# Optimization experiments

Measured on AMD Instinct MI355X. Metric: run time of the kernel, lower is better.

The kernel has to match this reference:

```python
import jax, jax.numpy as jnp
import numpy as np
import math

B, S, H, NH, HD, RD, INNER, MAXPOS, EPS = 2, 2048, 4096, 16, 256, 64, 16384, 2048, 1e-5


def setup_inputs() -> dict:
    key = jax.random.key(0)
    ks = jax.random.split(key, 8)
    sd = 0.02
    return {
        "hidden_states": jax.random.normal(ks[0], (B, S, H), jnp.float32),
        "attention_mask": jnp.ones((B, S), jnp.int32),
        "position_ids": jnp.broadcast_to(jnp.arange(S, dtype=jnp.int32), (B, S)),
        "ln_scale": jnp.ones((H,), jnp.float32),
        "ln_bias": jnp.zeros((H,), jnp.float32),
        "wq": jax.random.normal(ks[1], (H, H), jnp.float32) * sd,
        "wk": jax.random.normal(ks[2], (H, H), jnp.float32) * sd,
        "wv": jax.random.normal(ks[3], (H, H), jnp.float32) * sd,
        "wo": jax.random.normal(ks[4], (H, H), jnp.float32) * sd,
        "w_in": jax.random.normal(ks[5], (H, INNER), jnp.float32) * sd,
        "b_in": jnp.zeros((INNER,), jnp.float32),
        "w_out": jax.random.normal(ks[6], (INNER, H), jnp.float32) * sd,
        "b_out": jnp.zeros((H,), jnp.float32),
    }


def _rotate_every_two(t):
    # interleave (-odd, even) pairs along last dim
    r = jnp.stack((-t[..., 1::2], t[..., ::2]), axis=-1)
    return r.reshape(t.shape)


def reference(hidden_states, attention_mask, position_ids, ln_scale, ln_bias,
              wq, wk, wv, wo, w_in, b_in, w_out, b_out):
    x = hidden_states
    # LayerNorm (single ln feeds both attn and mlp in GPT-J parallel block)
    mu = jnp.mean(x, axis=-1, keepdims=True)
    var = jnp.mean(jnp.square(x - mu), axis=-1, keepdims=True)
    h = (x - mu) * jax.lax.rsqrt(var + EPS) * ln_scale + ln_bias

    # QKV projections (no bias), split heads: [B,S,NH,HD]
    q = (h @ wq).reshape(B, S, NH, HD)
    k = (h @ wk).reshape(B, S, NH, HD)
    v = (h @ wv).reshape(B, S, NH, HD)

    # sinusoidal table over rotary_dim, gathered by position_ids
    pos = jnp.arange(MAXPOS, dtype=jnp.float32)
    inv_freq = 1.0 / (10000.0 ** (jnp.arange(0, RD, 2, dtype=jnp.float32) / RD))
    freqs = pos[:, None] * inv_freq[None, :]          # [MAXPOS, RD//2]
    table = jnp.concatenate([jnp.sin(freqs), jnp.cos(freqs)], axis=-1)  # [MAXPOS, RD]
    sincos = table[position_ids]                      # [B,S,RD]
    sin, cos = jnp.split(sincos, 2, axis=-1)          # each [B,S,RD//2]
    sinr = jnp.repeat(sin[:, :, None, :], 2, axis=3)  # [B,S,1,RD]
    cosr = jnp.repeat(cos[:, :, None, :], 2, axis=3)

    def rope(t):
        return t * cosr + _rotate_every_two(t) * sinr

    q = jnp.concatenate([rope(q[..., :RD]), q[..., RD:]], axis=-1)
    k = jnp.concatenate([rope(k[..., :RD]), k[..., RD:]], axis=-1)

    # combined causal + padding mask -> additive bias
    causal = jnp.tril(jnp.ones((S, S), dtype=bool))
    mask = (attention_mask[:, None, None, :] > 0) & causal[None, None, :, :]
    bias = jnp.where(mask, 0.0, jnp.finfo(jnp.float32).min)  # [B,1,S,S]

    scale = 1.0 / math.sqrt(HD)
    scores = jnp.einsum('bqhd,bkhd->bhqk', q, k) * scale + bias
    attn = jax.nn.softmax(scores, axis=-1)
    ctx = jnp.einsum('bhqk,bkhd->bqhd', attn, v).reshape(B, S, H)
    attn_out = ctx @ wo

    # MLP on the same LN output (parallel residual), gelu_new ~ tanh gelu
    mlp = jax.nn.gelu(h @ w_in + b_in, approximate=True) @ w_out + b_out

    return x + attn_out + mlp
```

## Files before the change

### kernel.cpp

```cpp
#include <hip/hip_runtime.h>
#include <hip/hip_bf16.h>
#include <math.h>

namespace {

constexpr int kB = 2;
constexpr int kS = 2048;
constexpr int kH = 4096;
constexpr int kNH = 16;
constexpr int kHD = 256;

typedef __attribute__((ext_vector_type(4))) float f32x4;
typedef __attribute__((ext_vector_type(8))) short bf16x8;

__device__ __forceinline__ unsigned short f2bf(float f) {
  unsigned int u = __float_as_uint(f);
  u += 0x7FFFu + ((u >> 16) & 1u);
  return (unsigned short)(u >> 16);
}
__device__ __forceinline__ float bf2f(unsigned short h) {
  return __uint_as_float(((unsigned int)h) << 16);
}
__device__ __forceinline__ void gl2lds16(const void* g, void* l) {
  __builtin_amdgcn_global_load_lds(
      (const __attribute__((address_space(1))) unsigned int*)g,
      (__attribute__((address_space(3))) unsigned int*)l, 16, 0, 0);
}

__global__ __launch_bounds__(256) void ln_fwd(
    const float* __restrict__ x, const float* __restrict__ gam,
    const float* __restrict__ bet, unsigned short* __restrict__ hout,
    float* __restrict__ outp) {
  int row = blockIdx.x;
  int t = threadIdx.x;
  const float4* xr = (const float4*)(x + (size_t)row * kH);
  float4 v[4];
  float sum = 0.f, sq = 0.f;
#pragma unroll
  for (int i = 0; i < 4; i++) {
    v[i] = xr[t + i * 256];
    sum += v[i].x + v[i].y + v[i].z + v[i].w;
    sq += v[i].x * v[i].x + v[i].y * v[i].y + v[i].z * v[i].z + v[i].w * v[i].w;
  }
#pragma unroll
  for (int o = 32; o > 0; o >>= 1) {
    sum += __shfl_xor(sum, o);
    sq += __shfl_xor(sq, o);
  }
  __shared__ float red[8];
  if ((t & 63) == 0) { red[t >> 6] = sum; red[4 + (t >> 6)] = sq; }
  __syncthreads();
  sum = red[0] + red[1] + red[2] + red[3];
  sq = red[4] + red[5] + red[6] + red[7];
  float mu = sum * (1.f / kH);
  float rstd = rsqrtf(sq * (1.f / kH) - mu * mu + 1e-5f);
  const float4* gp = (const float4*)gam;
  const float4* bp = (const float4*)bet;
  ushort4* hr = (ushort4*)(hout + (size_t)row * kH);
  float4* orow = (float4*)(outp + (size_t)row * kH);
#pragma unroll
  for (int i = 0; i < 4; i++) {
    float4 g = gp[t + i * 256];
    float4 bb = bp[t + i * 256];
    ushort4 hv;
    hv.x = f2bf((v[i].x - mu) * rstd * g.x + bb.x);
    hv.y = f2bf((v[i].y - mu) * rstd * g.y + bb.y);
    hv.z = f2bf((v[i].z - mu) * rstd * g.z + bb.z);
    hv.w = f2bf((v[i].w - mu) * rstd * g.w + bb.w);
    hr[t + i * 256] = hv;
    orow[t + i * 256] = v[i];
  }
}

__global__ __launch_bounds__(256) void cvt_t(
    const float* __restrict__ in, int ldin, unsigned short* __restrict__ outp,
    int ldout) {
  __shared__ float tile[32][33];
  int n0 = blockIdx.x * 32, k0 = blockIdx.y * 32;
  int tx = threadIdx.x, ty = threadIdx.y;
#pragma unroll
  for (int i = 0; i < 4; i++)
    tile[ty + i * 8][tx] = in[(size_t)(k0 + ty + i * 8) * ldin + n0 + tx];
  __syncthreads();
#pragma unroll
  for (int i = 0; i < 4; i++)
    outp[(size_t)(n0 + ty + i * 8) * ldout + k0 + tx] =
        f2bf(tile[tx][ty + i * 8]);
}

__global__ __launch_bounds__(256) void vtrans(
    const unsigned short* __restrict__ v, unsigned short* __restrict__ vt) {
  __shared__ unsigned short tile[32][33];
  int bh = blockIdx.z;
  int s0 = blockIdx.x * 32, d0 = blockIdx.y * 32;
  int tx = threadIdx.x, ty = threadIdx.y;
  int b = bh >> 4, h = bh & 15;
  const unsigned short* src = v + (size_t)(b * kS) * kH + h * kHD;
#pragma unroll
  for (int i = 0; i < 4; i++)
    tile[ty + i * 8][tx] = src[(size_t)(s0 + ty + i * 8) * kH + d0 + tx];
  __syncthreads();
  unsigned short* dst = vt + (size_t)bh * kHD * kS;
#pragma unroll
  for (int i = 0; i < 4; i++)
    dst[(size_t)(d0 + ty + i * 8) * kS + s0 + tx] = tile[tx][ty + i * 8];
}

__global__ __launch_bounds__(256) void rope_scale(
    unsigned short* __restrict__ q, unsigned short* __restrict__ k,
    const int* __restrict__ pos) {
  int idx = blockIdx.x * 256 + threadIdx.x;
  int j = idx & 127;
  int rowh = idx >> 7;
  int h = rowh & 15;
  int s = (rowh >> 4) & 2047;
  int b = rowh >> 15;
  size_t off = ((size_t)(b * kS + s)) * kH + h * kHD + 2 * j;
  const float SCALE = 0.0625f;
  if (j < 32) {
    int p = pos[b * kS + s];
    float inv = exp2f(-(float)j * (13.287712379549449f / 32.f));
    float fr = (float)p * inv;
    float sn, cs;
    sincosf(fr, &sn, &cs);
    float e = bf2f(q[off]), o = bf2f(q[off + 1]);
    q[off] = f2bf((e * cs - o * sn) * SCALE);
    q[off + 1] = f2bf((o * cs + e * sn) * SCALE);
    e = bf2f(k[off]); o = bf2f(k[off + 1]);
    k[off] = f2bf(e * cs - o * sn);
    k[off + 1] = f2bf(o * cs + e * sn);
  } else {
    q[off] = f2bf(bf2f(q[off]) * SCALE);
    q[off + 1] = f2bf(bf2f(q[off + 1]) * SCALE);
  }
}

#define AF_MMA(P)                                                           \
  {                                                                         \
    bf16x8 af_[2][2];                                                       \
    _Pragma("unroll") for (int fm = 0; fm < 2; fm++)                        \
        _Pragma("unroll") for (int kk = 0; kk < 2; kk++) {                  \
      int q_ = (2 * (P) + fm) * 16 + l15;                                   \
      af_[fm][kk] = *(const bf16x8*)(cur + ((q_ & 64) << 8) + wm * 8192 +   \
                                     ((q_ & 63) << 7) +                     \
                                     ((((kk << 2) | l4) ^ key) << 4));      \
    }                                                                       \
    __builtin_amdgcn_s_setprio(1);                                          \
    _Pragma("unroll") for (int fm = 0; fm < 2; fm++)                        \
        _Pragma("unroll") for (int fn = 0; fn < 4; fn++)                    \
            _Pragma("unroll") for (int kk = 0; kk < 2; kk++)                \
      acc[2 * (P) + fm][fn] = __builtin_amdgcn_mfma_f32_16x16x32_bf16(      \
          af_[fm][kk], bfr[fn][kk], acc[2 * (P) + fm][fn], 0, 0, 0);        \
    __builtin_amdgcn_s_setprio(0);                                          \
  }

template <int EPI>
__global__ __launch_bounds__(512, 2) void gemm256(
    const unsigned short* __restrict__ A, int lda,
    const unsigned short* __restrict__ Bt, int ldb, void* __restrict__ Cp,
    int ldc, const float* __restrict__ bias, int K, int gx) {
  __shared__ __align__(16) char lds[131072];
  const int t = threadIdx.x;
  const int lane = t & 63, w = t >> 6;
  const int wm = w >> 2, wn = w & 3;
  const int l15 = lane & 15, l4 = lane >> 4;
  const int key = l15 & 7;

  const int nwg = gridDim.x;
  const int orig = blockIdx.x;
  const int wg = (orig & 7) * (nwg >> 3) + (orig >> 3);
  const int bx = wg % gx, by = wg / gx;
  const int m0 = by * 256, n0 = bx * 256;

  const int lr = t >> 3, ch = t & 7;
  const int swk = (ch ^ (lr & 7)) * 8;
  const unsigned short* aE0 = A + (size_t)(m0 + lr) * lda + swk;
  const unsigned short* aE1 = A + (size_t)(m0 + 128 + lr) * lda + swk;
  const unsigned short* aL0 = A + (size_t)(m0 + 64 + lr) * lda + swk;
  const unsigned short* aL1 = A + (size_t)(m0 + 192 + lr) * lda + swk;
  const unsigned short* b00 = Bt + (size_t)(n0 + lr) * ldb + swk;
  const unsigned short* b01 = Bt + (size_t)(n0 + 64 + lr) * ldb + swk;
  const unsigned short* b10 = Bt + (size_t)(n0 + 128 + lr) * ldb + swk;
  const unsigned short* b11 = Bt + (size_t)(n0 + 192 + lr) * ldb + swk;
  const int t16 = t * 16;

  f32x4 acc[8][4];
#pragma unroll
  for (int m = 0; m < 8; m++)
#pragma unroll
    for (int n = 0; n < 4; n++) acc[m][n] = (f32x4)(0.f);

  {
    char* b = lds;
    gl2lds16(b00, b + 32768 + t16); b00 += 64;
    gl2lds16(b01, b + 40960 + t16); b01 += 64;
    gl2lds16(b10, b + 49152 + t16); b10 += 64;
    gl2lds16(b11, b + 57344 + t16); b11 += 64;
    gl2lds16(aE0, b + t16);         aE0 += 64;
    gl2lds16(aE1, b + 8192 + t16);  aE1 += 64;
    gl2lds16(aL0, b + 16384 + t16); aL0 += 64;
    gl2lds16(aL1, b + 24576 + t16); aL1 += 64;
  }
  asm volatile("s_waitcnt vmcnt(2)" ::: "memory");
  asm volatile("s_barrier" ::: "memory");

  const int nt = K >> 6;
  for (int kt = 0; kt < nt; ++kt) {
    const char* cur = lds + (kt & 1) * 65536;
    char* nxt = lds + (((kt & 1) ^ 1)) * 65536;
    const bool pre = (kt + 1 < nt);
    bf16x8 bfr[4][2];
    if (pre) {
      gl2lds16(b00, nxt + 32768 + t16); b00 += 64;
      gl2lds16(b01, nxt + 40960 + t16); b01 += 64;
      gl2lds16(b10, nxt + 49152 + t16); b10 += 64;
      gl2lds16(b11, nxt + 57344 + t16); b11 += 64;
    }
#pragma unroll
    for (int fn = 0; fn < 4; fn++)
#pragma unroll
      for (int kk = 0; kk < 2; kk++) {
        int n = wn * 64 + fn * 16 + l15;
        bfr[fn][kk] = *(const bf16x8*)(cur + 32768 + (n << 7) +
                                       ((((kk << 2) | l4) ^ key) << 4));
      }
    AF_MMA(0)
    if (pre) {
      gl2lds16(aE0, nxt + t16);         aE0 += 64;
      gl2lds16(aE1, nxt + 8192 + t16);  aE1 += 64;
      gl2lds16(aL0, nxt + 16384 + t16); aL0 += 64;
      gl2lds16(aL1, nxt + 24576 + t16); aL1 += 64;
    }
    AF_MMA(1)
    if (pre) asm volatile("s_waitcnt vmcnt(8)" ::: "memory");
    else     asm volatile("s_waitcnt vmcnt(0)" ::: "memory");
    asm volatile("s_barrier" ::: "memory");
    AF_MMA(2)
    AF_MMA(3)
    asm volatile("s_waitcnt lgkmcnt(0)" ::: "memory");
    if (pre) asm volatile("s_waitcnt vmcnt(2)" ::: "memory");
    asm volatile("s_barrier" ::: "memory");
  }

  const int crow = m0 + wm * 128 + l4 * 4;
  const int ccol = n0 + wn * 64 + l15;
#pragma unroll
  for (int m = 0; m < 8; m++) {
#pragma unroll
    for (int n = 0; n < 4; n++) {
      int col = ccol + n * 16;
#pragma unroll
      for (int r = 0; r < 4; r++) {
        int row = crow + m * 16 + r;
        float v = acc[m][n][r];
        size_t idx = (size_t)row * ldc + col;
        if constexpr (EPI == 0) {
          ((unsigned short*)Cp)[idx] = f2bf(v);
        } else if constexpr (EPI == 1) {
          float u = v + bias[col];
          float c = 0.7978845608028654f * (u + 0.044715f * u * u * u);
          float g = u / (1.0f + __expf(-2.0f * c));
          ((unsigned short*)Cp)[idx] = f2bf(g);
        } else if constexpr (EPI == 2) {
          ((float*)Cp)[idx] += v;
        } else {
          ((float*)Cp)[idx] += v + bias[col];
        }
      }
    }
  }
}

__global__ __launch_bounds__(512) void attn_fwd(
    const unsigned short* __restrict__ q, const unsigned short* __restrict__ k,
    const unsigned short* __restrict__ vt, const int* __restrict__ amask,
    unsigned short* __restrict__ ctx) {
  __shared__ __align__(16) char alds[147456];
  const int t = threadIdx.x, lane = t & 63, w = t >> 6;
  const int bid = blockIdx.x;
  const int qb = 15 - (bid >> 5);
  const int bh = bid & 31;
  const int b = bh >> 4, h = bh & 15;
  const int l15 = lane & 15, l4 = lane >> 4;
  const int qbase = qb * 128;

  bf16x8 qf[8];
  {
    int qrow = qbase + w * 16 + l15;
    const unsigned short* qp =
        q + (size_t)(b * kS + qrow) * kH + h * kHD + l4 * 8;
#pragma unroll
    for (int ks = 0; ks < 8; ks++) qf[ks] = *(const bf16x8*)(qp + ks * 32);
  }
  f32x4 o[16];
#pragma unroll
  for (int nf = 0; nf < 16; nf++) o[nf] = (f32x4)(0.f);
  float mr[4] = {-INFINITY, -INFINITY, -INFINITY, -INFINITY};
  float lr[4] = {0.f, 0.f, 0.f, 0.f};

  const unsigned short* kbase = k + (size_t)(b * kS) * kH + h * kHD;
  const unsigned short* vbase = vt + (size_t)bh * kHD * kS;
  unsigned short* sPw = (unsigned short*)(alds + 131072 + w * 2048);
  const int nt = 2 * qb + 2;

  const int krow = t >> 5, kch = t & 31;
  const int kcs = (kch ^ (krow & 7)) * 8;
  const int vrow = t >> 3, vch = t & 7;
  const int vcs = (vch ^ (vrow & 7)) * 8;
  const int t16b = t * 16;

#define ATTN_STAGE(KV0, BUF)                                                 \
  {                                                                          \
    char* kd = alds + (BUF) * 32768;                                         \
    char* vd = alds + 65536 + (BUF) * 32768;                                 \
    _Pragma("unroll") for (int i = 0; i < 4; i++) {                          \
      gl2lds16(kbase + (size_t)((KV0) + krow + i * 16) * kH + kcs,           \
               kd + i * 8192 + t16b);                                        \
      gl2lds16(vbase + (size_t)(vrow + i * 64) * kS + (KV0) + vcs,           \
               vd + i * 8192 + t16b);                                        \
    }                                                                        \
  }

  ATTN_STAGE(0, 0)

  for (int kvt = 0; kvt < nt; kvt++) {
    const int kv0 = kvt * 64;
    const int cb = kvt & 1;
    if (kvt + 1 < nt) {
      ATTN_STAGE(kv0 + 64, cb ^ 1)
      asm volatile("s_waitcnt vmcnt(8)" ::: "memory");
    } else {
      asm volatile("s_waitcnt vmcnt(0)" ::: "memory");
    }
    asm volatile("s_barrier" ::: "memory");

    const unsigned short* sK = (const unsigned short*)(alds + cb * 32768);
    const unsigned short* sV =
        (const unsigned short*)(alds + 65536 + cb * 32768);

    f32x4 sc[4];
#pragma unroll
    for (int g = 0; g < 4; g++) sc[g] = (f32x4)(0.f);
    __builtin_amdgcn_s_setprio(1);
#pragma unroll
    for (int g = 0; g < 4; g++) {
      int row = g * 16 + l15;
#pragma unroll
      for (int ks = 0; ks < 8; ks++) {
        bf16x8 kf =
            *(const bf16x8*)&sK[row * 256 + (((ks * 4 + l4) ^ (row & 7)) * 8)];
        sc[g] = __builtin_amdgcn_mfma_f32_16x16x32_bf16(qf[ks], kf, sc[g], 0, 0, 0);
      }
    }
    __builtin_amdgcn_s_setprio(0);

    int am[4];
#pragma unroll
    for (int g = 0; g < 4; g++) am[g] = amask[b * kS + kv0 + g * 16 + l15];
    float mx[4];
#pragma unroll
    for (int r = 0; r < 4; r++) {
      int qi = qbase + w * 16 + l4 * 4 + r;
      float a = -INFINITY;
#pragma unroll
      for (int g = 0; g < 4; g++) {
        bool ok = (kv0 + g * 16 + l15 <= qi) && (am[g] != 0);
        float s = ok ? sc[g][r] : -INFINITY;
        sc[g][r] = s;
        a = fmaxf(a, s);
      }
#pragma unroll
      for (int d = 1; d < 16; d <<= 1) a = fmaxf(a, __shfl_xor(a, d));
      mx[r] = a;
    }
    bool nd = false;
#pragma unroll
    for (int r = 0; r < 4; r++) nd |= (mx[r] > mr[r] + 8.f);
    if (__any(nd)) {
#pragma unroll
      for (int r = 0; r < 4; r++) {
        float nm = fmaxf(mr[r], mx[r]);
        float c = __expf(mr[r] - nm);
        lr[r] *= c;
        mr[r] = nm;
#pragma unroll
        for (int nf = 0; nf < 16; nf++) o[nf][r] *= c;
      }
    }
#pragma unroll
    for (int r = 0; r < 4; r++) {
      int prow = l4 * 4 + r;
      int pkey = (prow ^ (prow >> 2)) & 7;
      float rs = 0.f;
#pragma unroll
      for (int g = 0; g < 4; g++) {
        float p = __expf(sc[g][r] - mr[r]);
        rs += p;
        int kvl = g * 16 + l15;
        sPw[prow * 64 + (((kvl >> 3) ^ pkey) << 3) + (kvl & 7)] = f2bf(p);
      }
#pragma unroll
      for (int d = 1; d < 16; d <<= 1) rs += __shfl_xor(rs, d);
      lr[r] += rs;
    }
    asm volatile("s_waitcnt lgkmcnt(0)" ::: "memory");

    int rkey = (l15 ^ (l15 >> 2)) & 7;
    bf16x8 pa[2];
#pragma unroll
    for (int ks2 = 0; ks2 < 2; ks2++)
      pa[ks2] = *(const bf16x8*)&sPw[l15 * 64 + (((ks2 * 4 + l4) ^ rkey) << 3)];
    __builtin_amdgcn_s_setprio(1);
#pragma unroll
    for (int nf = 0; nf < 16; nf++) {
      int vr = nf * 16 + l15;
#pragma unroll
      for (int ks2 = 0; ks2 < 2; ks2++) {
        bf16x8 vf =
            *(const bf16x8*)&sV[vr * 64 + (((ks2 * 4 + l4) ^ (vr & 7)) * 8)];
        o[nf] = __builtin_amdgcn_mfma_f32_16x16x32_bf16(pa[ks2], vf, o[nf], 0, 0, 0);
      }
    }
    __builtin_amdgcn_s_setprio(0);
    asm volatile("s_barrier" ::: "memory");
  }

  float invl[4];
#pragma unroll
  for (int r = 0; r < 4; r++) invl[r] = 1.0f / lr[r];
#pragma unroll
  for (int nf = 0; nf < 16; nf++) {
    int d = nf * 16 + l15;
#pragma unroll
    for (int r = 0; r < 4; r++) {
      int qi = qbase + w * 16 + l4 * 4 + r;
      ctx[(size_t)(b * kS + qi) * kH + h * kHD + d] = f2bf(o[nf][r] * invl[r]);
    }
  }
#undef ATTN_STAGE
}

}

extern "C" void kernel_launch(void* const* d_in, const int* in_sizes, int n_in,
                              void* d_out, int out_size, void* d_ws,
                              size_t ws_size, hipStream_t stream) {
  const float* x = (const float*)d_in[0];
  const int* amask = (const int*)d_in[1];
  const int* pos = (const int*)d_in[2];
  const float* lns = (const float*)d_in[3];
  const float* lnb = (const float*)d_in[4];
  const float* wq = (const float*)d_in[5];
  const float* wk = (const float*)d_in[6];
  const float* wv = (const float*)d_in[7];
  const float* wo = (const float*)d_in[8];
  const float* w_in = (const float*)d_in[9];
  const float* b_in = (const float*)d_in[10];
  const float* w_out = (const float*)d_in[11];
  const float* b_out = (const float*)d_in[12];
  float* out = (float*)d_out;

  if (ws_size < 268435456ull) return;
  char* ws = (char*)d_ws;
  unsigned short* h_bf = (unsigned short*)ws;
  unsigned short* big = (unsigned short*)(ws + 33554432ull);
  unsigned short* vbuf = (unsigned short*)(ws + 167772160ull);
  unsigned short* wbuf = (unsigned short*)(ws + 201326592ull);
  unsigned short* mid = big;
  unsigned short* qbuf = big;
  unsigned short* kbuf = big + 16777216;
  unsigned short* vtb = big + 33554432;
  unsigned short* ctxb = vbuf;

  dim3 t256(256);
  dim3 t512(512);
  dim3 t32x8(32, 8);

  ln_fwd<<<kB * kS, t256, 0, stream>>>(x, lns, lnb, h_bf, out);

  for (int c = 0; c < 2; c++) {
    cvt_t<<<dim3(256, 128), t32x8, 0, stream>>>(w_in + c * 8192, 16384, wbuf, 4096);
    gemm256<1><<<dim3(512), t512, 0, stream>>>(
        h_bf, 4096, wbuf, 4096, mid + c * 8192, 16384, b_in + c * 8192, 4096, 32);
  }
  for (int c = 0; c < 2; c++) {
    cvt_t<<<dim3(128, 256), t32x8, 0, stream>>>(
        w_out + (size_t)c * 8192 * 4096, 4096, wbuf, 8192);
    if (c == 0)
      gemm256<3><<<dim3(256), t512, 0, stream>>>(mid + c * 8192, 16384, wbuf,
                                                 8192, out, 4096, b_out, 8192, 16);
    else
      gemm256<2><<<dim3(256), t512, 0, stream>>>(
          mid + c * 8192, 16384, wbuf, 8192, out, 4096, nullptr, 8192, 16);
  }

  const float* wqkv[3] = {wq, wk, wv};
  unsigned short* qkvp[3] = {qbuf, kbuf, vbuf};
  for (int i = 0; i < 3; i++) {
    cvt_t<<<dim3(128, 128), t32x8, 0, stream>>>(wqkv[i], 4096, wbuf, 4096);
    gemm256<0><<<dim3(256), t512, 0, stream>>>(h_bf, 4096, wbuf, 4096,
                                               qkvp[i], 4096, nullptr, 4096, 16);
  }
  rope_scale<<<32768, t256, 0, stream>>>(qbuf, kbuf, pos);
  vtrans<<<dim3(64, 8, 32), t32x8, 0, stream>>>(vbuf, vtb);
  attn_fwd<<<dim3(512), t512, 0, stream>>>(qbuf, kbuf, vtb, amask, ctxb);
  cvt_t<<<dim3(128, 128), t32x8, 0, stream>>>(wo, 4096, wbuf, 4096);
  gemm256<2><<<dim3(256), t512, 0, stream>>>(ctxb, 4096, wbuf, 4096, out,
                                             4096, nullptr, 4096, 16);
}
```

Before: 2.005 ms.

## Replace 256x256 GEMM with 256x128 tile, K=32 triple-buffered pipeline

Rewrites the bf16 MFMA GEMM to use 256x128 output tiles with a 32-wide K step and a three-stage LDS ring buffer loaded via global_load_lds. The wave layout becomes 4x2, each wave holding a 4x4 accumulator grid, and LDS drops to about 72KB so four blocks can target each CU. All GEMM launches double their grid counts to match. The aim is more occupancy, more blocks per GEMM and deeper prefetch; in exchange, operand reuse per tile is lower and there is a barrier every 32-wide K step.

```diff
diff --git a/kernel.cpp b/kernel.cpp
--- a/kernel.cpp
+++ b/kernel.cpp
@@ -26,6 +26,9 @@
       (const __attribute__((address_space(1))) unsigned int*)g,
       (__attribute__((address_space(3))) unsigned int*)l, 16, 0, 0);
 }
+
+#define SBAR asm volatile("s_barrier" ::: "memory")
+#define LGKM0 asm volatile("s_waitcnt lgkmcnt(0)" ::: "memory")
 
 __global__ __launch_bounds__(256) void ln_fwd(
     const float* __restrict__ x, const float* __restrict__ gam,
@@ -135,117 +138,88 @@
   }
 }
 
-#define AF_MMA(P)                                                           \
-  {                                                                         \
-    bf16x8 af_[2][2];                                                       \
-    _Pragma("unroll") for (int fm = 0; fm < 2; fm++)                        \
-        _Pragma("unroll") for (int kk = 0; kk < 2; kk++) {                  \
-      int q_ = (2 * (P) + fm) * 16 + l15;                                   \
-      af_[fm][kk] = *(const bf16x8*)(cur + ((q_ & 64) << 8) + wm * 8192 +   \
-                                     ((q_ & 63) << 7) +                     \
-                                     ((((kk << 2) | l4) ^ key) << 4));      \
-    }                                                                       \
-    __builtin_amdgcn_s_setprio(1);                                          \
-    _Pragma("unroll") for (int fm = 0; fm < 2; fm++)                        \
-        _Pragma("unroll") for (int fn = 0; fn < 4; fn++)                    \
-            _Pragma("unroll") for (int kk = 0; kk < 2; kk++)                \
-      acc[2 * (P) + fm][fn] = __builtin_amdgcn_mfma_f32_16x16x32_bf16(      \
-          af_[fm][kk], bfr[fn][kk], acc[2 * (P) + fm][fn], 0, 0, 0);        \
-    __builtin_amdgcn_s_setprio(0);                                          \
-  }
-
 template <int EPI>
-__global__ __launch_bounds__(512, 2) void gemm256(
+__global__ __launch_bounds__(512, 4) void gemmk(
     const unsigned short* __restrict__ A, int lda,
     const unsigned short* __restrict__ Bt, int ldb, void* __restrict__ Cp,
     int ldc, const float* __restrict__ bias, int K, int gx) {
-  __shared__ __align__(16) char lds[131072];
+  __shared__ __align__(16) char lds[73728];
   const int t = threadIdx.x;
   const int lane = t & 63, w = t >> 6;
-  const int wm = w >> 2, wn = w & 3;
+  const int wm = w >> 1, wn = w & 1;
   const int l15 = lane & 15, l4 = lane >> 4;
-  const int key = l15 & 7;
 
   const int nwg = gridDim.x;
   const int orig = blockIdx.x;
   const int wg = (orig & 7) * (nwg >> 3) + (orig >> 3);
   const int bx = wg % gx, by = wg / gx;
-  const int m0 = by * 256, n0 = bx * 256;
-
-  const int lr = t >> 3, ch = t & 7;
-  const int swk = (ch ^ (lr & 7)) * 8;
-  const unsigned short* aE0 = A + (size_t)(m0 + lr) * lda + swk;
-  const unsigned short* aE1 = A + (size_t)(m0 + 128 + lr) * lda + swk;
-  const unsigned short* aL0 = A + (size_t)(m0 + 64 + lr) * lda + swk;
-  const unsigned short* aL1 = A + (size_t)(m0 + 192 + lr) * lda + swk;
-  const unsigned short* b00 = Bt + (size_t)(n0 + lr) * ldb + swk;
-  const unsigned short* b01 = Bt + (size_t)(n0 + 64 + lr) * ldb + swk;
-  const unsigned short* b10 = Bt + (size_t)(n0 + 128 + lr) * ldb + swk;
-  const unsigned short* b11 = Bt + (size_t)(n0 + 192 + lr) * ldb + swk;
+  const int m0 = by * 256, n0 = bx * 128;
+
+  const int lr = t >> 2, ch = t & 3;
+  const int swo = ((ch ^ ((lr & 3) ^ ((lr >> 2) & 3))) << 3);
+  const unsigned short* aS0 = A + (size_t)(m0 + lr) * lda + swo;
+  const unsigned short* aS1 = A + (size_t)(m0 + 128 + lr) * lda + swo;
+  const unsigned short* bS = Bt + (size_t)(n0 + lr) * ldb + swo;
   const int t16 = t * 16;
 
-  f32x4 acc[8][4];
-#pragma unroll
-  for (int m = 0; m < 8; m++)
+  const int keyR = (l15 & 3) ^ ((l15 >> 2) & 3);
+  const int rch = ((l4 ^ keyR) << 4);
+  const int abase = wm * 4096 + l15 * 64 + rch;
+  const int bbase = 16384 + wn * 4096 + l15 * 64 + rch;
+
+  f32x4 acc[4][4];
+#pragma unroll
+  for (int m = 0; m < 4; m++)
 #pragma unroll
     for (int n = 0; n < 4; n++) acc[m][n] = (f32x4)(0.f);
 
-  {
-    char* b = lds;
-    gl2lds16(b00, b + 32768 + t16); b00 += 64;
-    gl2lds16(b01, b + 40960 + t16); b01 += 64;
-    gl2lds16(b10, b + 49152 + t16); b10 += 64;
-    gl2lds16(b11, b + 57344 + t16); b11 += 64;
-    gl2lds16(aE0, b + t16);         aE0 += 64;
-    gl2lds16(aE1, b + 8192 + t16);  aE1 += 64;
-    gl2lds16(aL0, b + 16384 + t16); aL0 += 64;
-    gl2lds16(aL1, b + 24576 + t16); aL1 += 64;
-  }
-  asm volatile("s_waitcnt vmcnt(2)" ::: "memory");
-  asm volatile("s_barrier" ::: "memory");
-
-  const int nt = K >> 6;
+  gl2lds16(aS0, lds + t16);
+  gl2lds16(aS1, lds + 8192 + t16);
+  gl2lds16(bS, lds + 16384 + t16);
+  aS0 += 32; aS1 += 32; bS += 32;
+  gl2lds16(aS0, lds + 24576 + t16);
+  gl2lds16(aS1, lds + 24576 + 8192 + t16);
+  gl2lds16(bS, lds + 24576 + 16384 + t16);
+  aS0 += 32; aS1 += 32; bS += 32;
+  asm volatile("s_waitcnt vmcnt(3)" ::: "memory");
+  SBAR;
+
+  int offR = 0, off1 = 24576, offW = 49152;
+  const int nt = K >> 5;
   for (int kt = 0; kt < nt; ++kt) {
-    const char* cur = lds + (kt & 1) * 65536;
-    char* nxt = lds + (((kt & 1) ^ 1)) * 65536;
-    const bool pre = (kt + 1 < nt);
-    bf16x8 bfr[4][2];
-    if (pre) {
-      gl2lds16(b00, nxt + 32768 + t16); b00 += 64;
-      gl2lds16(b01, nxt + 40960 + t16); b01 += 64;
-      gl2lds16(b10, nxt + 49152 + t16); b10 += 64;
-      gl2lds16(b11, nxt + 57344 + t16); b11 += 64;
-    }
-#pragma unroll
-    for (int fn = 0; fn < 4; fn++)
-#pragma unroll
-      for (int kk = 0; kk < 2; kk++) {
-        int n = wn * 64 + fn * 16 + l15;
-        bfr[fn][kk] = *(const bf16x8*)(cur + 32768 + (n << 7) +
-                                       ((((kk << 2) | l4) ^ key) << 4));
-      }
-    AF_MMA(0)
-    if (pre) {
-      gl2lds16(aE0, nxt + t16);         aE0 += 64;
-      gl2lds16(aE1, nxt + 8192 + t16);  aE1 += 64;
-      gl2lds16(aL0, nxt + 16384 + t16); aL0 += 64;
-      gl2lds16(aL1, nxt + 24576 + t16); aL1 += 64;
-    }
-    AF_MMA(1)
-    if (pre) asm volatile("s_waitcnt vmcnt(8)" ::: "memory");
-    else     asm volatile("s_waitcnt vmcnt(0)" ::: "memory");
-    asm volatile("s_barrier" ::: "memory");
-    AF_MMA(2)
-    AF_MMA(3)
-    asm volatile("s_waitcnt lgkmcnt(0)" ::: "memory");
-    if (pre) asm volatile("s_waitcnt vmcnt(2)" ::: "memory");
-    asm volatile("s_barrier" ::: "memory");
-  }
-
-  const int crow = m0 + wm * 128 + l4 * 4;
+    if (kt + 2 < nt) {
+      gl2lds16(aS0, lds + offW + t16);
+      gl2lds16(aS1, lds + offW + 8192 + t16);
+      gl2lds16(bS, lds + offW + 16384 + t16);
+      aS0 += 32; aS1 += 32; bS += 32;
+    }
+    const char* cur = lds + offR;
+    bf16x8 af[4], bv[4];
+#pragma unroll
+    for (int m = 0; m < 4; m++)
+      af[m] = *(const bf16x8*)(cur + abase + m * 1024);
+#pragma unroll
+    for (int n = 0; n < 4; n++)
+      bv[n] = *(const bf16x8*)(cur + bbase + n * 1024);
+    __builtin_amdgcn_s_setprio(1);
+#pragma unroll
+    for (int m = 0; m < 4; m++)
+#pragma unroll
+      for (int n = 0; n < 4; n++)
+        acc[m][n] = __builtin_amdgcn_mfma_f32_16x16x32_bf16(af[m], bv[n],
+                                                            acc[m][n], 0, 0, 0);
+    __builtin_amdgcn_s_setprio(0);
+    LGKM0;
+    if (kt + 2 < nt) asm volatile("s_waitcnt vmcnt(3)" ::: "memory");
+    else             asm volatile("s_waitcnt vmcnt(0)" ::: "memory");
+    SBAR;
+    int tmp = offR; offR = off1; off1 = offW; offW = tmp;
+  }
+
+  const int crow = m0 + wm * 64 + l4 * 4;
   const int ccol = n0 + wn * 64 + l15;
 #pragma unroll
-  for (int m = 0; m < 8; m++) {
+  for (int m = 0; m < 4; m++) {
 #pragma unroll
     for (int n = 0; n < 4; n++) {
       int col = ccol + n * 16;
@@ -480,31 +454,31 @@
 
   for (int c = 0; c < 2; c++) {
     cvt_t<<<dim3(256, 128), t32x8, 0, stream>>>(w_in + c * 8192, 16384, wbuf, 4096);
-    gemm256<1><<<dim3(512), t512, 0, stream>>>(
-        h_bf, 4096, wbuf, 4096, mid + c * 8192, 16384, b_in + c * 8192, 4096, 32);
+    gemmk<1><<<dim3(1024), t512, 0, stream>>>(
+        h_bf, 4096, wbuf, 4096, mid + c * 8192, 16384, b_in + c * 8192, 4096, 64);
   }
   for (int c = 0; c < 2; c++) {
     cvt_t<<<dim3(128, 256), t32x8, 0, stream>>>(
         w_out + (size_t)c * 8192 * 4096, 4096, wbuf, 8192);
     if (c == 0)
-      gemm256<3><<<dim3(256), t512, 0, stream>>>(mid + c * 8192, 16384, wbuf,
-                                                 8192, out, 4096, b_out, 8192, 16);
+      gemmk<3><<<dim3(512), t512, 0, stream>>>(mid + c * 8192, 16384, wbuf,
+                                               8192, out, 4096, b_out, 8192, 32);
     else
-      gemm256<2><<<dim3(256), t512, 0, stream>>>(
-          mid + c * 8192, 16384, wbuf, 8192, out, 4096, nullptr, 8192, 16);
+      gemmk<2><<<dim3(512), t512, 0, stream>>>(
+          mid + c * 8192, 16384, wbuf, 8192, out, 4096, nullptr, 8192, 32);
   }
 
   const float* wqkv[3] = {wq, wk, wv};
   unsigned short* qkvp[3] = {qbuf, kbuf, vbuf};
   for (int i = 0; i < 3; i++) {
     cvt_t<<<dim3(128, 128), t32x8, 0, stream>>>(wqkv[i], 4096, wbuf, 4096);
-    gemm256<0><<<dim3(256), t512, 0, stream>>>(h_bf, 4096, wbuf, 4096,
-                                               qkvp[i], 4096, nullptr, 4096, 16);
+    gemmk<0><<<dim3(512), t512, 0, stream>>>(h_bf, 4096, wbuf, 4096,
+                                             qkvp[i], 4096, nullptr, 4096, 32);
   }
   rope_scale<<<32768, t256, 0, stream>>>(qbuf, kbuf, pos);
   vtrans<<<dim3(64, 8, 32), t32x8, 0, stream>>>(vbuf, vtb);
   attn_fwd<<<dim3(512), t512, 0, stream>>>(qbuf, kbuf, vtb, amask, ctxb);
   cvt_t<<<dim3(128, 128), t32x8, 0, stream>>>(wo, 4096, wbuf, 4096);
-  gemm256<2><<<dim3(256), t512, 0, stream>>>(ctxb, 4096, wbuf, 4096, out,
-                                             4096, nullptr, 4096, 16);
-}
+  gemmk<2><<<dim3(512), t512, 0, stream>>>(ctxb, 4096, wbuf, 4096, out,
+                                           4096, nullptr, 4096, 32);
+}
```

New measurement: 2.342 ms. +16.8%, slower.

## Fuse QKV projections into one GEMM and merge MLP down-projection chunks

Applied to the files above, without the earlier changes.

The three separate Q/K/V GEMMs are replaced by one GEMM over a concatenated transposed weight, writing into an interleaved QKV buffer with row stride 12288. The rope, V-transpose and attention kernels are updated to read from that strided buffer. The MLP down-projection now runs as a single K=16384 GEMM instead of two K=8192 passes that each re-read and accumulate into the fp32 output. The attention path is reordered to run before the MLP, and the workspace is reassigned so buffers alias across phases. The goal is fewer launches, better wave fill on the larger grids, and less output read-modify-write traffic. The cost is larger weight conversions and more careful buffer lifetime management.

```diff
diff --git a/kernel.cpp b/kernel.cpp
--- a/kernel.cpp
+++ b/kernel.cpp
@@ -9,6 +9,7 @@
 constexpr int kH = 4096;
 constexpr int kNH = 16;
 constexpr int kHD = 256;
+constexpr int kLDQ = 12288;
 
 typedef __attribute__((ext_vector_type(4))) float f32x4;
 typedef __attribute__((ext_vector_type(8))) short bf16x8;
@@ -26,6 +27,9 @@
       (const __attribute__((address_space(1))) unsigned int*)g,
       (__attribute__((address_space(3))) unsigned int*)l, 16, 0, 0);
 }
+
+#define SBAR asm volatile("s_barrier" ::: "memory")
+#define LGKM0 asm volatile("s_waitcnt lgkmcnt(0)" ::: "memory")
 
 __global__ __launch_bounds__(256) void ln_fwd(
     const float* __restrict__ x, const float* __restrict__ gam,
@@ -89,16 +93,17 @@
 }
 
 __global__ __launch_bounds__(256) void vtrans(
-    const unsigned short* __restrict__ v, unsigned short* __restrict__ vt) {
+    const unsigned short* __restrict__ qkv, unsigned short* __restrict__ vt) {
   __shared__ unsigned short tile[32][33];
   int bh = blockIdx.z;
   int s0 = blockIdx.x * 32, d0 = blockIdx.y * 32;
   int tx = threadIdx.x, ty = threadIdx.y;
   int b = bh >> 4, h = bh & 15;
-  const unsigned short* src = v + (size_t)(b * kS) * kH + h * kHD;
+  const unsigned short* src =
+      qkv + (size_t)(b * kS) * kLDQ + 8192 + h * kHD;
 #pragma unroll
   for (int i = 0; i < 4; i++)
-    tile[ty + i * 8][tx] = src[(size_t)(s0 + ty + i * 8) * kH + d0 + tx];
+    tile[ty + i * 8][tx] = src[(size_t)(s0 + ty + i * 8) * kLDQ + d0 + tx];
   __syncthreads();
   unsigned short* dst = vt + (size_t)bh * kHD * kS;
 #pragma unroll
@@ -107,15 +112,14 @@
 }
 
 __global__ __launch_bounds__(256) void rope_scale(
-    unsigned short* __restrict__ q, unsigned short* __restrict__ k,
-    const int* __restrict__ pos) {
+    unsigned short* __restrict__ qkv, const int* __restrict__ pos) {
   int idx = blockIdx.x * 256 + threadIdx.x;
   int j = idx & 127;
   int rowh = idx >> 7;
   int h = rowh & 15;
   int s = (rowh >> 4) & 2047;
   int b = rowh >> 15;
-  size_t off = ((size_t)(b * kS + s)) * kH + h * kHD + 2 * j;
+  size_t off = ((size_t)(b * kS + s)) * kLDQ + h * kHD + 2 * j;
   const float SCALE = 0.0625f;
   if (j < 32) {
     int p = pos[b * kS + s];
@@ -123,15 +127,15 @@
     float fr = (float)p * inv;
     float sn, cs;
     sincosf(fr, &sn, &cs);
-    float e = bf2f(q[off]), o = bf2f(q[off + 1]);
-    q[off] = f2bf((e * cs - o * sn) * SCALE);
-    q[off + 1] = f2bf((o * cs + e * sn) * SCALE);
-    e = bf2f(k[off]); o = bf2f(k[off + 1]);
-    k[off] = f2bf(e * cs - o * sn);
-    k[off + 1] = f2bf(o * cs + e * sn);
+    float e = bf2f(qkv[off]), o = bf2f(qkv[off + 1]);
+    qkv[off] = f2bf((e * cs - o * sn) * SCALE);
+    qkv[off + 1] = f2bf((o * cs + e * sn) * SCALE);
+    e = bf2f(qkv[off + 4096]); o = bf2f(qkv[off + 4097]);
+    qkv[off + 4096] = f2bf(e * cs - o * sn);
+    qkv[off + 4097] = f2bf(o * cs + e * sn);
   } else {
-    q[off] = f2bf(bf2f(q[off]) * SCALE);
-    q[off + 1] = f2bf(bf2f(q[off + 1]) * SCALE);
+    qkv[off] = f2bf(bf2f(qkv[off]) * SCALE);
+    qkv[off + 1] = f2bf(bf2f(qkv[off + 1]) * SCALE);
   }
 }
 
@@ -202,7 +206,7 @@
     gl2lds16(aL1, b + 24576 + t16); aL1 += 64;
   }
   asm volatile("s_waitcnt vmcnt(2)" ::: "memory");
-  asm volatile("s_barrier" ::: "memory");
+  SBAR;
 
   const int nt = K >> 6;
   for (int kt = 0; kt < nt; ++kt) {
@@ -234,12 +238,12 @@
     AF_MMA(1)
     if (pre) asm volatile("s_waitcnt vmcnt(8)" ::: "memory");
     else     asm volatile("s_waitcnt vmcnt(0)" ::: "memory");
-    asm volatile("s_barrier" ::: "memory");
+    SBAR;
     AF_MMA(2)
     AF_MMA(3)
-    asm volatile("s_waitcnt lgkmcnt(0)" ::: "memory");
+    LGKM0;
     if (pre) asm volatile("s_waitcnt vmcnt(2)" ::: "memory");
-    asm volatile("s_barrier" ::: "memory");
+    SBAR;
   }
 
   const int crow = m0 + wm * 128 + l4 * 4;
@@ -272,9 +276,8 @@
 }
 
 __global__ __launch_bounds__(512) void attn_fwd(
-    const unsigned short* __restrict__ q, const unsigned short* __restrict__ k,
-    const unsigned short* __restrict__ vt, const int* __restrict__ amask,
-    unsigned short* __restrict__ ctx) {
+    const unsigned short* __restrict__ qkv, const unsigned short* __restrict__ vt,
+    const int* __restrict__ amask, unsigned short* __restrict__ ctx) {
   __shared__ __align__(16) char alds[147456];
   const int t = threadIdx.x, lane = t & 63, w = t >> 6;
   const int bid = blockIdx.x;
@@ -288,7 +291,7 @@
   {
     int qrow = qbase + w * 16 + l15;
     const unsigned short* qp =
-        q + (size_t)(b * kS + qrow) * kH + h * kHD + l4 * 8;
+        qkv + (size_t)(b * kS + qrow) * kLDQ + h * kHD + l4 * 8;
 #pragma unroll
     for (int ks = 0; ks < 8; ks++) qf[ks] = *(const bf16x8*)(qp + ks * 32);
   }
@@ -298,7 +301,8 @@
   float mr[4] = {-INFINITY, -INFINITY, -INFINITY, -INFINITY};
   float lr[4] = {0.f, 0.f, 0.f, 0.f};
 
-  const unsigned short* kbase = k + (size_t)(b * kS) * kH + h * kHD;
+  const unsigned short* kbase =
+      qkv + (size_t)(b * kS) * kLDQ + 4096 + h * kHD;
   const unsigned short* vbase = vt + (size_t)bh * kHD * kS;
   unsigned short* sPw = (unsigned short*)(alds + 131072 + w * 2048);
   const int nt = 2 * qb + 2;
@@ -314,7 +318,7 @@
     char* kd = alds + (BUF) * 32768;                                         \
     char* vd = alds + 65536 + (BUF) * 32768;                                 \
     _Pragma("unroll") for (int i = 0; i < 4; i++) {                          \
-      gl2lds16(kbase + (size_t)((KV0) + krow + i * 16) * kH + kcs,           \
+      gl2lds16(kbase + (size_t)((KV0) + krow + i * 16) * kLDQ + kcs,         \
                kd + i * 8192 + t16b);                                        \
       gl2lds16(vbase + (size_t)(vrow + i * 64) * kS + (KV0) + vcs,           \
                vd + i * 8192 + t16b);                                        \
@@ -461,16 +465,16 @@
   float* out = (float*)d_out;
 
   if (ws_size < 268435456ull) return;
-  char* ws = (char*)d_ws;
-  unsigned short* h_bf = (unsigned short*)ws;
-  unsigned short* big = (unsigned short*)(ws + 33554432ull);
-  unsigned short* vbuf = (unsigned short*)(ws + 167772160ull);
-  unsigned short* wbuf = (unsigned short*)(ws + 201326592ull);
-  unsigned short* mid = big;
-  unsigned short* qbuf = big;
-  unsigned short* kbuf = big + 16777216;
-  unsigned short* vtb = big + 33554432;
-  unsigned short* ctxb = vbuf;
+  unsigned short* ws = (unsigned short*)d_ws;
+  unsigned short* h_bf = ws;
+  unsigned short* wqkvT = ws + 16777216;
+  unsigned short* qkv = ws + 67108864;
+  unsigned short* vtb = ws + 117440512;
+  unsigned short* ctxb = ws + 16777216;
+  unsigned short* woT = ws + 33554432;
+  unsigned short* w_inT = ws + 33554432;
+  unsigned short* mid = ws + 67108864;
+  unsigned short* w_outT = ws;
 
   dim3 t256(256);
   dim3 t512(512);
@@ -478,33 +482,25 @@
 
   ln_fwd<<<kB * kS, t256, 0, stream>>>(x, lns, lnb, h_bf, out);
 
+  cvt_t<<<dim3(128, 128), t32x8, 0, stream>>>(wq, 4096, wqkvT, 4096);
+  cvt_t<<<dim3(128, 128), t32x8, 0, stream>>>(wk, 4096, wqkvT + 16777216, 4096);
+  cvt_t<<<dim3(128, 128), t32x8, 0, stream>>>(wv, 4096, wqkvT + 33554432, 4096);
+  gemm256<0><<<dim3(768), t512, 0, stream>>>(h_bf, 4096, wqkvT, 4096,
+                                             qkv, kLDQ, nullptr, 4096, 48);
+  rope_scale<<<32768, t256, 0, stream>>>(qkv, pos);
+  vtrans<<<dim3(64, 8, 32), t32x8, 0, stream>>>(qkv, vtb);
+  attn_fwd<<<dim3(512), t512, 0, stream>>>(qkv, vtb, amask, ctxb);
+  cvt_t<<<dim3(128, 128), t32x8, 0, stream>>>(wo, 4096, woT, 4096);
+  gemm256<2><<<dim3(256), t512, 0, stream>>>(ctxb, 4096, woT, 4096, out,
+                                             4096, nullptr, 4096, 16);
   for (int c = 0; c < 2; c++) {
-    cvt_t<<<dim3(256, 128), t32x8, 0, stream>>>(w_in + c * 8192, 16384, wbuf, 4096);
+    cvt_t<<<dim3(256, 128), t32x8, 0, stream>>>(w_in + c * 8192, 16384, w_inT,
+                                                4096);
     gemm256<1><<<dim3(512), t512, 0, stream>>>(
-        h_bf, 4096, wbuf, 4096, mid + c * 8192, 16384, b_in + c * 8192, 4096, 32);
-  }
-  for (int c = 0; c < 2; c++) {
-    cvt_t<<<dim3(128, 256), t32x8, 0, stream>>>(
-        w_out + (size_t)c * 8192 * 4096, 4096, wbuf, 8192);
-    if (c == 0)
-      gemm256<3><<<dim3(256), t512, 0, stream>>>(mid + c * 8192, 16384, wbuf,
-                                                 8192, out, 4096, b_out, 8192, 16);
-    else
-      gemm256<2><<<dim3(256), t512, 0, stream>>>(
-          mid + c * 8192, 16384, wbuf, 8192, out, 4096, nullptr, 8192, 16);
-  }
-
-  const float* wqkv[3] = {wq, wk, wv};
-  unsigned short* qkvp[3] = {qbuf, kbuf, vbuf};
-  for (int i = 0; i < 3; i++) {
-    cvt_t<<<dim3(128, 128), t32x8, 0, stream>>>(wqkv[i], 4096, wbuf, 4096);
-    gemm256<0><<<dim3(256), t512, 0, stream>>>(h_bf, 4096, wbuf, 4096,
-                                               qkvp[i], 4096, nullptr, 4096, 16);
-  }
-  rope_scale<<<32768, t256, 0, stream>>>(qbuf, kbuf, pos);
-  vtrans<<<dim3(64, 8, 32), t32x8, 0, stream>>>(vbuf, vtb);
-  attn_fwd<<<dim3(512), t512, 0, stream>>>(qbuf, kbuf, vtb, amask, ctxb);
-  cvt_t<<<dim3(128, 128), t32x8, 0, stream>>>(wo, 4096, wbuf, 4096);
-  gemm256<2><<<dim3(256), t512, 0, stream>>>(ctxb, 4096, wbuf, 4096, out,
-                                             4096, nullptr, 4096, 16);
-}
+        h_bf, 4096, w_inT, 4096, mid + c * 8192, 16384, b_in + c * 8192, 4096,
+        32);
+  }
+  cvt_t<<<dim3(128, 512), t32x8, 0, stream>>>(w_out, 4096, w_outT, 16384);
+  gemm256<3><<<dim3(256), t512, 0, stream>>>(mid, 16384, w_outT, 16384, out,
+                                             4096, b_out, 16384, 16);
+}
```

New measurement: 1.945 ms (median of 2 runs). -3.0%, faster.
